# Kernel tuning notes

Measured on AMD Instinct MI355X. Metric: run time of the kernel, lower is better.

## Reference

```python
import jax, jax.numpy as jnp
import numpy as np
from jax import lax

C, H, W, N = 128, 48, 48, 16
SHIFT_W = 1   # frozen value of p_3_1_1 (random.randint(-3,3) in original)
SHIFT_C = 1   # frozen value of p_11_0_1


def setup_inputs() -> dict:
    key = jax.random.key(0)
    k1, k2, k3, k4, k5 = jax.random.split(key, 5)
    x = jax.random.normal(k1, (N, C, H, W), dtype=jnp.float32)
    # p_5_w: trunc_normal std=0.02, shape (1,c,h,w)
    p5_w = 0.02 * jax.random.truncated_normal(k2, -2.0, 2.0, (1, C, H, W), dtype=jnp.float32)
    # p_6: 1x1 conv c->c, no bias -> weight (c, c)
    w6 = jax.random.normal(k3, (C, C), dtype=jnp.float32) / np.float32(np.sqrt(C))
    # p_8: Conv2d(1, c//2, (1,5), dilation=(1,3), padding=(0,6), bias=False)
    w8 = jax.random.normal(k4, (C // 2, 1, 1, 5), dtype=jnp.float32) / np.float32(np.sqrt(5))
    # p_10: 1x1 conv 3c/2 -> c, no bias
    w10 = jax.random.normal(k5, (C, 3 * C // 2), dtype=jnp.float32) / np.float32(np.sqrt(3 * C // 2))
    return {"x": x, "p5_w": p5_w, "w6": w6, "w8": w8, "w10": w10}


def _forward(x, p5_w, w6, w8, w10):
    n, c, h, w = x.shape
    hw = h * w
    inv_sqrt_c = np.float32(1.0 / np.sqrt(c))
    inv_sqrt_hw = np.float32(1.0 / np.sqrt(hw))

    t1 = x.max(axis=1)                                    # (n,h,w) channel max
    t2 = -x
    t4 = jnp.maximum(t2, jnp.roll(t2, SHIFT_W, axis=3))    # roll along width
    t5 = p5_w * t4
    t6 = jnp.einsum('oc,nchw->nohw', w6, t5)               # 1x1 conv p_6

    # score tensor t_7: (n, hw, hw)
    t7 = jnp.einsum('ncp,ncq->npq', t6.reshape(n, c, hw), x.reshape(n, c, hw)) * inv_sqrt_c

    # dilated 1x5 conv on channel-max map
    t8 = lax.conv_general_dilated(
        t1[:, None, :, :], w8, window_strides=(1, 1),
        padding=((0, 0), (6, 6)), rhs_dilation=(1, 3),
        dimension_numbers=('NCHW', 'OIHW', 'NCHW'))        # (n, c/2, h, w)

    # unfold kernel (3,1), dilation (2,1), padding (2,0): rows i-2, i, i+2
    pad = jnp.pad(t8, ((0, 0), (0, 0), (2, 2), (0, 0)))
    t9 = jnp.stack([pad[:, :, 2 * k:2 * k + h, :] for k in range(3)], axis=2)  # (n,c/2,3,h,w)

    t10 = jnp.einsum('oc,nchw->nohw', w10, t9.reshape(n, 3 * c // 2, h, w))   # 1x1 conv p_10
    t11 = jnp.roll(t10, SHIFT_C, axis=1)                   # roll along channels
    t12 = jnp.maximum(x, t11)

    # out[n,q,c] = sum_p t7[n,p,q] * t12[n,c,p]
    t13 = jnp.einsum('npq,ncp->nqc', t7, t12.reshape(n, c, hw)) * inv_sqrt_hw
    return t13.reshape(n, h, w, c).transpose(0, 3, 1, 2)   # (n,c,h,w)


def reference(x, p5_w, w6, w8, w10):
    return _forward(x, p5_w, w6, w8, w10)
```

## Files before the change

### kernel.cpp

```cpp
#include <hip/hip_runtime.h>
#include <cmath>

typedef short bf16x8 __attribute__((ext_vector_type(8)));
typedef short bf16x4 __attribute__((ext_vector_type(4)));
typedef float f32x4 __attribute__((ext_vector_type(4)));

namespace {
constexpr int kN   = 16;
constexpr int kC   = 128;
constexpr int kH   = 48;
constexpr int kW   = 48;
constexpr int kHW  = kH * kW;
constexpr int kK9  = 192;
constexpr int kNPC = 18;
constexpr int kPCH = kHW / kNPC;
constexpr int kLS  = 132;
constexpr int kPA  = 136;
}

__device__ __forceinline__ unsigned short f2b(float f) {
  unsigned u = __builtin_bit_cast(unsigned, f);
  u = (u + 0x7FFFu + ((u >> 16) & 1u)) >> 16;
  return (unsigned short)u;
}
__device__ __forceinline__ float b2f(unsigned short u) {
  return __builtin_bit_cast(float, ((unsigned)u) << 16);
}

__device__ __forceinline__ int tidx(int w, int c) {
  return w * kLS + (c ^ (((w >> 2) & 3) << 3));
}

__global__ __launch_bounds__(256)
void k_prep(const float* __restrict__ p5, const float* __restrict__ w6,
            const float* __restrict__ w10, const float* __restrict__ w8,
            float* __restrict__ p5T, unsigned short* __restrict__ w6b,
            float* __restrict__ Weff) {
  const int tid = threadIdx.x;
  const int bb = blockIdx.x;
  if (bb < 48) {
    __shared__ float Ls[kW * kLS];
    const int h = bb;
    for (int i = 0; i < 6; ++i) {
      const int idx = i * 256 + tid;
      const int c = idx / 12, s = idx % 12;
      const float4 v = *(const float4*)(p5 + (size_t)c * kHW + h * kW + s * 4);
      const int sw = (s & 3) << 3;
      Ls[(4 * s + 0) * kLS + (c ^ sw)] = v.x;
      Ls[(4 * s + 1) * kLS + (c ^ sw)] = v.y;
      Ls[(4 * s + 2) * kLS + (c ^ sw)] = v.z;
      Ls[(4 * s + 3) * kLS + (c ^ sw)] = v.w;
    }
    __syncthreads();
    for (int i = 0; i < 3; ++i) {
      const int idx = i * 256 + tid;
      const int w = idx >> 4, c = (idx & 15) * 8;
      const float* s = &Ls[tidx(w, c)];
      float4 a{s[0], s[1], s[2], s[3]}, b{s[4], s[5], s[6], s[7]};
      float* dst = p5T + ((size_t)(h * kW + w)) * kC + c;
      *(float4*)dst = a;
      *(float4*)(dst + 4) = b;
    }
  } else if (bb < 112) {
    const int i = (bb - 48) * 256 + tid;
    w6b[i] = f2b(w6[i]);
  } else {
    const int idx = (bb - 112) * 256 + tid;
    if (idx < kC * 15) {
      const int o = idx / 15, t = idx - o * 15;
      const int kk = t / 5, j = t - kk * 5;
      float s = 0.f;
#pragma unroll
      for (int c2 = 0; c2 < 64; ++c2)
        s = fmaf(w10[o * kK9 + 3 * c2 + kk], w8[c2 * 5 + j], s);
      Weff[idx] = s;
    }
  }
}

__global__ __launch_bounds__(256)
void k_xt5t6(const float* __restrict__ x, const float* __restrict__ p5T,
             const unsigned short* __restrict__ w6b,
             unsigned short* __restrict__ xT, unsigned short* __restrict__ xB,
             float* __restrict__ t1, unsigned short* __restrict__ t6) {
  __shared__ __align__(16) float Ls[kW * kLS];
  __shared__ __align__(16) unsigned short w6s[kC * kPA];
  __shared__ __align__(16) unsigned short t5s[kW * kPA];
  const int b = blockIdx.x;
  const int n = b / kH, h = b - n * kH;
  const int tid = threadIdx.x;
  const float* xrow = x + (size_t)n * kC * kHW + h * kW;
  unsigned short* xBrow = xB + (size_t)n * kC * kHW + h * kW;
  for (int i = 0; i < 6; ++i) {
    const int idx = i * 256 + tid;
    const int c = idx / 12, s = idx % 12;
    const float4 v = *(const float4*)(xrow + (size_t)c * kHW + s * 4);
    const int sw = (s & 3) << 3;
    Ls[(4 * s + 0) * kLS + (c ^ sw)] = v.x;
    Ls[(4 * s + 1) * kLS + (c ^ sw)] = v.y;
    Ls[(4 * s + 2) * kLS + (c ^ sw)] = v.z;
    Ls[(4 * s + 3) * kLS + (c ^ sw)] = v.w;
    bf16x4 xb4{(short)f2b(v.x), (short)f2b(v.y), (short)f2b(v.z), (short)f2b(v.w)};
    *(bf16x4*)(xBrow + (size_t)c * kHW + s * 4) = xb4;
  }
  for (int i = 0; i < 8; ++i) {
    const int f = i * 256 + tid;
    const int o = f >> 4, seg = (f & 15) * 8;
    *(bf16x8*)&w6s[o * kPA + seg] = *(const bf16x8*)(w6b + o * kC + seg);
  }
  __syncthreads();

  for (int i = 0; i < 3; ++i) {
    const int idx = i * 256 + tid;
    const int w = idx >> 4, c = (idx & 15) * 8;
    const int wp = (w == 0) ? (kW - 1) : (w - 1);
    const float* sv = &Ls[tidx(w, c)];
    const float* sp = &Ls[tidx(wp, c)];
    const int q = h * kW + w;
    const float* pv = p5T + (size_t)q * kC + c;

    unsigned short xb[8], tb[8];
    float m = -3.4e38f;
#pragma unroll
    for (int j = 0; j < 8; ++j) {
      const float xv = sv[j];
      const float t5 = pv[j] * fmaxf(-xv, -sp[j]);
      xb[j] = f2b(xv);
      tb[j] = f2b(t5);
      m = fmaxf(m, xv);
    }
    *(bf16x8*)(xT + ((size_t)n * kHW + q) * kC + c) = *(const bf16x8*)xb;
    *(bf16x8*)&t5s[w * kPA + c] = *(const bf16x8*)tb;
#pragma unroll
    for (int off = 1; off < 16; off <<= 1)
      m = fmaxf(m, __shfl_xor(m, off, 16));
    if ((tid & 15) == 0) t1[(size_t)n * kHW + q] = m;
  }
  __syncthreads();

  const int wv = tid >> 6, lane = tid & 63;
  const int lr = lane & 15, lk = (lane >> 4) * 8;
  f32x4 acc[2][3];
#pragma unroll
  for (int i = 0; i < 2; ++i)
#pragma unroll
    for (int j = 0; j < 3; ++j) acc[i][j] = f32x4{0.f, 0.f, 0.f, 0.f};
#pragma unroll
  for (int ks = 0; ks < kC; ks += 32) {
    bf16x8 a[2], bf[3];
#pragma unroll
    for (int mt = 0; mt < 2; ++mt)
      a[mt] = *(const bf16x8*)&w6s[(32 * wv + 16 * mt + lr) * kPA + ks + lk];
#pragma unroll
    for (int nt = 0; nt < 3; ++nt)
      bf[nt] = *(const bf16x8*)&t5s[(16 * nt + lr) * kPA + ks + lk];
#pragma unroll
    for (int mt = 0; mt < 2; ++mt)
#pragma unroll
      for (int nt = 0; nt < 3; ++nt)
        acc[mt][nt] = __builtin_amdgcn_mfma_f32_16x16x32_bf16(a[mt], bf[nt], acc[mt][nt], 0, 0, 0);
  }
#pragma unroll
  for (int mt = 0; mt < 2; ++mt)
#pragma unroll
    for (int nt = 0; nt < 3; ++nt) {
      const int q = h * kW + 16 * nt + lr;
#pragma unroll
      for (int r = 0; r < 4; ++r) {
        const int o = 32 * wv + 16 * mt + 4 * (lane >> 4) + r;
        t6[((size_t)n * kC + o) * kHW + q] = f2b(acc[mt][nt][r]);
      }
    }
}

__global__ __launch_bounds__(256)
void k_corr(const unsigned short* __restrict__ xB, const float* __restrict__ t1,
            const float* __restrict__ Weff, const unsigned short* __restrict__ t6,
            float* __restrict__ part) {
  __shared__ __align__(16) unsigned short t12s[kC * kPA];
  __shared__ __align__(16) unsigned short Bsf[kC * kPA];
  __shared__ __align__(16) float t1s[8 * 60];
  __shared__ float sW[kC][15];
  const int tid = threadIdx.x;
  const int n = blockIdx.y;
  const int p0 = blockIdx.x * kPCH;
  const int h_lo = p0 / kW;
  const unsigned short* Bg = t6 + (size_t)n * kC * kHW + p0;

  for (int i = tid; i < 8 * 60; i += 256) {
    const int r = i / 60, cc = i - r * 60;
    const int hh = h_lo - 2 + r, ww = cc - 6;
    t1s[i] = (hh >= 0 && hh < kH && ww >= 0 && ww < kW) ? t1[n * kHW + hh * kW + ww] : 0.f;
  }
  for (int i = tid; i < kC * 15; i += 256) {
    const int c = i / 15, t = i - c * 15;
    sW[c][t] = Weff[((c - 1) & (kC - 1)) * 15 + t];
  }
#pragma unroll
  for (int i = 0; i < 8; ++i) {
    const int f = i * 256 + tid;
    const int c = f >> 4, seg = (f & 15) * 8;
    *(bf16x8*)&Bsf[c * kPA + seg] = *(const bf16x8*)(Bg + (size_t)c * kHW + seg);
  }
  __syncthreads();

  const unsigned short* xn = xB + (size_t)n * kC * kHW;
  for (int it = 0; it < 8; ++it) {
    const int idx = it * 256 + tid;
    const int c = idx >> 4, p = (idx & 15) * 8;
    const int q = p0 + p;
    const int h = q / kW, w0 = q - h * kW;
    const int r0 = h - h_lo;
    float tap[3][20];
#pragma unroll
    for (int kk = 0; kk < 3; ++kk) {
      const float* src = &t1s[(r0 + 2 * kk) * 60 + w0];
#pragma unroll
      for (int j4 = 0; j4 < 5; ++j4) {
        const float4 v = *(const float4*)(src + 4 * j4);
        tap[kk][4 * j4 + 0] = v.x; tap[kk][4 * j4 + 1] = v.y;
        tap[kk][4 * j4 + 2] = v.z; tap[kk][4 * j4 + 3] = v.w;
      }
    }
    float wr[15];
#pragma unroll
    for (int t = 0; t < 15; ++t) wr[t] = sW[c][t];
    const bf16x8 xv8 = *(const bf16x8*)(xn + (size_t)c * kHW + q);
    unsigned short o16[8];
#pragma unroll
    for (int dp = 0; dp < 8; ++dp) {
      float acc = 0.f;
#pragma unroll
      for (int kk = 0; kk < 3; ++kk)
#pragma unroll
        for (int j = 0; j < 5; ++j)
          acc = fmaf(wr[kk * 5 + j], tap[kk][3 * j + dp], acc);
      o16[dp] = f2b(fmaxf(b2f((unsigned short)xv8[dp]), acc));
    }
    *(bf16x8*)&t12s[c * kPA + p] = *(const bf16x8*)o16;
  }
  __syncthreads();

  const int wv = tid >> 6, lane = tid & 63;
  const int lr = lane & 15, lk = (lane >> 4) * 8;
  const int wr2 = (wv >> 1) * 64, wc2 = (wv & 1) * 64;
  f32x4 acc[4][4];
#pragma unroll
  for (int i = 0; i < 4; ++i)
#pragma unroll
    for (int j = 0; j < 4; ++j) acc[i][j] = f32x4{0.f, 0.f, 0.f, 0.f};

#pragma unroll
  for (int ks = 0; ks < kPCH; ks += 32) {
    bf16x8 a[4], bv[4];
#pragma unroll
    for (int i = 0; i < 4; ++i) {
      a[i]  = *(const bf16x8*)&t12s[(wr2 + 16 * i + lr) * kPA + ks + lk];
      bv[i] = *(const bf16x8*)&Bsf[(wc2 + 16 * i + lr) * kPA + ks + lk];
    }
#pragma unroll
    for (int i = 0; i < 4; ++i)
#pragma unroll
      for (int j = 0; j < 4; ++j)
        acc[i][j] = __builtin_amdgcn_mfma_f32_16x16x32_bf16(a[i], bv[j], acc[i][j], 0, 0, 0);
  }

  float* dst = part + ((size_t)blockIdx.x * kN + n) * (kC * kC);
#pragma unroll
  for (int i = 0; i < 4; ++i)
#pragma unroll
    for (int j = 0; j < 4; ++j)
#pragma unroll
      for (int r = 0; r < 4; ++r)
        dst[(wr2 + 16 * i + 4 * (lane >> 4) + r) * kC + wc2 + 16 * j + lr] = acc[i][j][r];
}

__global__ __launch_bounds__(256)
void k_redM(const float* __restrict__ part, unsigned short* __restrict__ M) {
  const int idx = blockIdx.x * 256 + threadIdx.x;
  const int n = idx >> 14, r = idx & 16383;
  float s = 0.f;
#pragma unroll
  for (int ch = 0; ch < kNPC; ++ch)
    s += part[(((size_t)ch * kN + n) << 14) + r];
  M[idx] = f2b(s);
}

__global__ __launch_bounds__(256)
void k_out(const unsigned short* __restrict__ A, const unsigned short* __restrict__ B,
           float* __restrict__ Out, float scale) {
  constexpr int K = 128;
  __shared__ __align__(16) unsigned short As[kC * kPA];
  __shared__ __align__(16) unsigned short Bs[64 * kPA];
  const int tid = threadIdx.x;
  const int n = blockIdx.y;
  const int qbase = blockIdx.x * 64;
  const unsigned short* Ag = A + (size_t)n * kC * K;
  const unsigned short* Bg = B + ((size_t)n * kHW + qbase) * K;

  {
    const int m = tid >> 1, hf = tid & 1;
    const unsigned short* src = Ag + (size_t)m * K + hf * 64;
    unsigned short* dst = &As[m * kPA + hf * 64];
#pragma unroll
    for (int i = 0; i < 8; ++i)
      *(bf16x8*)(dst + 8 * i) = *(const bf16x8*)(src + 8 * i);
  }
#pragma unroll
  for (int i = 0; i < 4; ++i) {
    const int f = i * 256 + tid;
    const int q = f >> 4, seg = (f & 15) * 8;
    *(bf16x8*)&Bs[q * kPA + seg] = *(const bf16x8*)(Bg + (size_t)q * K + seg);
  }
  __syncthreads();

  const int wv = tid >> 6, lane = tid & 63;
  const int lr = lane & 15, lk = (lane >> 4) * 8;

  f32x4 acc[2][4];
#pragma unroll
  for (int i = 0; i < 2; ++i)
#pragma unroll
    for (int j = 0; j < 4; ++j) acc[i][j] = f32x4{0.f, 0.f, 0.f, 0.f};

#pragma unroll
  for (int ks = 0; ks < K; ks += 32) {
    bf16x8 a[2], b[4];
#pragma unroll
    for (int mt = 0; mt < 2; ++mt)
      a[mt] = *(const bf16x8*)&As[(32 * wv + 16 * mt + lr) * kPA + ks + lk];
#pragma unroll
    for (int nt = 0; nt < 4; ++nt)
      b[nt] = *(const bf16x8*)&Bs[(16 * nt + lr) * kPA + ks + lk];
#pragma unroll
    for (int mt = 0; mt < 2; ++mt)
#pragma unroll
      for (int nt = 0; nt < 4; ++nt)
        acc[mt][nt] = __builtin_amdgcn_mfma_f32_16x16x32_bf16(
            a[mt], b[nt], acc[mt][nt], 0, 0, 0);
  }

#pragma unroll
  for (int mt = 0; mt < 2; ++mt)
#pragma unroll
    for (int nt = 0; nt < 4; ++nt) {
      const int q = qbase + 16 * nt + lr;
#pragma unroll
      for (int r = 0; r < 4; ++r) {
        const int m = 32 * wv + 16 * mt + 4 * (lane >> 4) + r;
        Out[((size_t)n * kC + m) * kHW + q] = scale * acc[mt][nt][r];
      }
    }
}

extern "C" void kernel_launch(void* const* d_in, const int* in_sizes, int n_in,
                              void* d_out, int out_size, void* d_ws, size_t ws_size,
                              hipStream_t stream) {
  const float* x   = (const float*)d_in[0];
  const float* p5  = (const float*)d_in[1];
  const float* w6  = (const float*)d_in[2];
  const float* w8  = (const float*)d_in[3];
  const float* w10 = (const float*)d_in[4];
  float* out = (float*)d_out;

  char* ws = (char*)d_ws;
  unsigned short* xT   = (unsigned short*)(ws);
  unsigned short* t6b  = (unsigned short*)(ws + 9437184);
  float*          part = (float*)(ws + 18874368);
  unsigned short* xB   = (unsigned short*)(ws + 37748736);
  unsigned short* Mb   = (unsigned short*)(ws + 47185920);
  float*          t1b  = (float*)(ws + 47710208);
  unsigned short* w6b  = (unsigned short*)(ws + 47857664);
  float*          Weff = (float*)(ws + 47890432);
  float*          p5T  = (float*)(ws + 47898112);

  const float scale = 1.0f / (sqrtf((float)kC) * sqrtf((float)kHW));

  k_prep<<<120, 256, 0, stream>>>(p5, w6, w10, w8, p5T, w6b, Weff);
  k_xt5t6<<<kN * kH, 256, 0, stream>>>(x, p5T, w6b, xT, xB, t1b, t6b);
  k_corr<<<dim3(kNPC, kN), 256, 0, stream>>>(xB, t1b, Weff, t6b, part);
  k_redM<<<kN * kC * kC / 256, 256, 0, stream>>>(part, Mb);
  k_out<<<dim3(kHW / 64, kN), 256, 0, stream>>>(Mb, xT, out, scale);
}
```

Measured before the change: 50.12 us.

## Fold prep kernel into first stage, store partials as bf16, remap block order

Removes the separate prep kernel. The first stage now converts w6 to bf16 itself, computes t5 directly from the coalesced x and p5 row loads, and has block 0 compute Weff. Correlation partial sums are stored as bf16 instead of fp32, and the reduction reads them as 8-wide vectors. Grids are flattened with n as the fastest-varying block index, which changes which blocks run together and how they share the cache. Bf16 partials halve the traffic for partials but add rounding error before the sum. Having block 0 compute Weff inside the same kernel is only safe because Weff is consumed by the next launch.

```diff
diff --git a/kernel.cpp b/kernel.cpp
--- a/kernel.cpp
+++ b/kernel.cpp
@@ -32,41 +32,21 @@
 }
 
 __global__ __launch_bounds__(256)
-void k_prep(const float* __restrict__ p5, const float* __restrict__ w6,
-            const float* __restrict__ w10, const float* __restrict__ w8,
-            float* __restrict__ p5T, unsigned short* __restrict__ w6b,
-            float* __restrict__ Weff) {
+void k_xt5t6(const float* __restrict__ x, const float* __restrict__ p5,
+             const float* __restrict__ w6, const float* __restrict__ w10,
+             const float* __restrict__ w8,
+             unsigned short* __restrict__ xT, unsigned short* __restrict__ xB,
+             float* __restrict__ t1, unsigned short* __restrict__ t6,
+             float* __restrict__ Weff) {
+  __shared__ __align__(16) float Ls[kW * kLS];
+  __shared__ __align__(16) unsigned short w6s[kC * kPA];
+  __shared__ __align__(16) unsigned short t5s[kW * kPA];
+  const int bid = blockIdx.x;
+  const int h = bid >> 4, n = bid & 15;
   const int tid = threadIdx.x;
-  const int bb = blockIdx.x;
-  if (bb < 48) {
-    __shared__ float Ls[kW * kLS];
-    const int h = bb;
-    for (int i = 0; i < 6; ++i) {
-      const int idx = i * 256 + tid;
-      const int c = idx / 12, s = idx % 12;
-      const float4 v = *(const float4*)(p5 + (size_t)c * kHW + h * kW + s * 4);
-      const int sw = (s & 3) << 3;
-      Ls[(4 * s + 0) * kLS + (c ^ sw)] = v.x;
-      Ls[(4 * s + 1) * kLS + (c ^ sw)] = v.y;
-      Ls[(4 * s + 2) * kLS + (c ^ sw)] = v.z;
-      Ls[(4 * s + 3) * kLS + (c ^ sw)] = v.w;
-    }
-    __syncthreads();
-    for (int i = 0; i < 3; ++i) {
-      const int idx = i * 256 + tid;
-      const int w = idx >> 4, c = (idx & 15) * 8;
-      const float* s = &Ls[tidx(w, c)];
-      float4 a{s[0], s[1], s[2], s[3]}, b{s[4], s[5], s[6], s[7]};
-      float* dst = p5T + ((size_t)(h * kW + w)) * kC + c;
-      *(float4*)dst = a;
-      *(float4*)(dst + 4) = b;
-    }
-  } else if (bb < 112) {
-    const int i = (bb - 48) * 256 + tid;
-    w6b[i] = f2b(w6[i]);
-  } else {
-    const int idx = (bb - 112) * 256 + tid;
-    if (idx < kC * 15) {
+
+  if (bid == 0) {
+    for (int idx = tid; idx < kC * 15; idx += 256) {
       const int o = idx / 15, t = idx - o * 15;
       const int kk = t / 5, j = t - kk * 5;
       float s = 0.f;
@@ -76,25 +56,17 @@
       Weff[idx] = s;
     }
   }
-}
-
-__global__ __launch_bounds__(256)
-void k_xt5t6(const float* __restrict__ x, const float* __restrict__ p5T,
-             const unsigned short* __restrict__ w6b,
-             unsigned short* __restrict__ xT, unsigned short* __restrict__ xB,
-             float* __restrict__ t1, unsigned short* __restrict__ t6) {
-  __shared__ __align__(16) float Ls[kW * kLS];
-  __shared__ __align__(16) unsigned short w6s[kC * kPA];
-  __shared__ __align__(16) unsigned short t5s[kW * kPA];
-  const int b = blockIdx.x;
-  const int n = b / kH, h = b - n * kH;
-  const int tid = threadIdx.x;
+
   const float* xrow = x + (size_t)n * kC * kHW + h * kW;
+  const float* prow = p5 + h * kW;
   unsigned short* xBrow = xB + (size_t)n * kC * kHW + h * kW;
+
   for (int i = 0; i < 6; ++i) {
     const int idx = i * 256 + tid;
     const int c = idx / 12, s = idx % 12;
     const float4 v = *(const float4*)(xrow + (size_t)c * kHW + s * 4);
+    const float xm1 = xrow[(size_t)c * kHW + ((s == 0) ? (kW - 1) : (s * 4 - 1))];
+    const float4 pv = *(const float4*)(prow + (size_t)c * kHW + s * 4);
     const int sw = (s & 3) << 3;
     Ls[(4 * s + 0) * kLS + (c ^ sw)] = v.x;
     Ls[(4 * s + 1) * kLS + (c ^ sw)] = v.y;
@@ -102,35 +74,40 @@
     Ls[(4 * s + 3) * kLS + (c ^ sw)] = v.w;
     bf16x4 xb4{(short)f2b(v.x), (short)f2b(v.y), (short)f2b(v.z), (short)f2b(v.w)};
     *(bf16x4*)(xBrow + (size_t)c * kHW + s * 4) = xb4;
+    const float t50 = pv.x * fmaxf(-v.x, -xm1);
+    const float t51 = pv.y * fmaxf(-v.y, -v.x);
+    const float t52 = pv.z * fmaxf(-v.z, -v.y);
+    const float t53 = pv.w * fmaxf(-v.w, -v.z);
+    t5s[(4 * s + 0) * kPA + c] = f2b(t50);
+    t5s[(4 * s + 1) * kPA + c] = f2b(t51);
+    t5s[(4 * s + 2) * kPA + c] = f2b(t52);
+    t5s[(4 * s + 3) * kPA + c] = f2b(t53);
   }
   for (int i = 0; i < 8; ++i) {
     const int f = i * 256 + tid;
     const int o = f >> 4, seg = (f & 15) * 8;
-    *(bf16x8*)&w6s[o * kPA + seg] = *(const bf16x8*)(w6b + o * kC + seg);
+    const float4 a = *(const float4*)(w6 + (size_t)o * kC + seg);
+    const float4 b = *(const float4*)(w6 + (size_t)o * kC + seg + 4);
+    bf16x8 w8v{(short)f2b(a.x), (short)f2b(a.y), (short)f2b(a.z), (short)f2b(a.w),
+               (short)f2b(b.x), (short)f2b(b.y), (short)f2b(b.z), (short)f2b(b.w)};
+    *(bf16x8*)&w6s[o * kPA + seg] = w8v;
   }
   __syncthreads();
 
   for (int i = 0; i < 3; ++i) {
     const int idx = i * 256 + tid;
     const int w = idx >> 4, c = (idx & 15) * 8;
-    const int wp = (w == 0) ? (kW - 1) : (w - 1);
     const float* sv = &Ls[tidx(w, c)];
-    const float* sp = &Ls[tidx(wp, c)];
     const int q = h * kW + w;
-    const float* pv = p5T + (size_t)q * kC + c;
-
-    unsigned short xb[8], tb[8];
+    unsigned short xb[8];
     float m = -3.4e38f;
 #pragma unroll
     for (int j = 0; j < 8; ++j) {
       const float xv = sv[j];
-      const float t5 = pv[j] * fmaxf(-xv, -sp[j]);
       xb[j] = f2b(xv);
-      tb[j] = f2b(t5);
       m = fmaxf(m, xv);
     }
     *(bf16x8*)(xT + ((size_t)n * kHW + q) * kC + c) = *(const bf16x8*)xb;
-    *(bf16x8*)&t5s[w * kPA + c] = *(const bf16x8*)tb;
 #pragma unroll
     for (int off = 1; off < 16; off <<= 1)
       m = fmaxf(m, __shfl_xor(m, off, 16));
@@ -176,14 +153,15 @@
 __global__ __launch_bounds__(256)
 void k_corr(const unsigned short* __restrict__ xB, const float* __restrict__ t1,
             const float* __restrict__ Weff, const unsigned short* __restrict__ t6,
-            float* __restrict__ part) {
+            unsigned short* __restrict__ part) {
   __shared__ __align__(16) unsigned short t12s[kC * kPA];
   __shared__ __align__(16) unsigned short Bsf[kC * kPA];
   __shared__ __align__(16) float t1s[8 * 60];
   __shared__ float sW[kC][15];
+  const int bid = blockIdx.x;
+  const int chunk = bid >> 4, n = bid & 15;
   const int tid = threadIdx.x;
-  const int n = blockIdx.y;
-  const int p0 = blockIdx.x * kPCH;
+  const int p0 = chunk * kPCH;
   const int h_lo = p0 / kW;
   const unsigned short* Bg = t6 + (size_t)n * kC * kHW + p0;
 
@@ -265,25 +243,34 @@
         acc[i][j] = __builtin_amdgcn_mfma_f32_16x16x32_bf16(a[i], bv[j], acc[i][j], 0, 0, 0);
   }
 
-  float* dst = part + ((size_t)blockIdx.x * kN + n) * (kC * kC);
+  unsigned short* dst = part + ((size_t)chunk * kN + n) * (kC * kC);
 #pragma unroll
   for (int i = 0; i < 4; ++i)
 #pragma unroll
     for (int j = 0; j < 4; ++j)
 #pragma unroll
       for (int r = 0; r < 4; ++r)
-        dst[(wr2 + 16 * i + 4 * (lane >> 4) + r) * kC + wc2 + 16 * j + lr] = acc[i][j][r];
+        dst[(wr2 + 16 * i + 4 * (lane >> 4) + r) * kC + wc2 + 16 * j + lr] = f2b(acc[i][j][r]);
 }
 
 __global__ __launch_bounds__(256)
-void k_redM(const float* __restrict__ part, unsigned short* __restrict__ M) {
-  const int idx = blockIdx.x * 256 + threadIdx.x;
-  const int n = idx >> 14, r = idx & 16383;
-  float s = 0.f;
-#pragma unroll
-  for (int ch = 0; ch < kNPC; ++ch)
-    s += part[(((size_t)ch * kN + n) << 14) + r];
-  M[idx] = f2b(s);
+void k_redM(const unsigned short* __restrict__ part, unsigned short* __restrict__ M) {
+  const int bid = blockIdx.x;
+  const int j = bid >> 4, n = bid & 15;
+  const int r0 = (j * 256 + threadIdx.x) * 8;
+  float acc[8];
+#pragma unroll
+  for (int e = 0; e < 8; ++e) acc[e] = 0.f;
+#pragma unroll
+  for (int ch = 0; ch < kNPC; ++ch) {
+    const bf16x8 v = *(const bf16x8*)(part + (((size_t)ch * kN + n) << 14) + r0);
+#pragma unroll
+    for (int e = 0; e < 8; ++e) acc[e] += b2f((unsigned short)v[e]);
+  }
+  unsigned short o16[8];
+#pragma unroll
+  for (int e = 0; e < 8; ++e) o16[e] = f2b(acc[e]);
+  *(bf16x8*)(M + ((size_t)n << 14) + r0) = *(const bf16x8*)o16;
 }
 
 __global__ __launch_bounds__(256)
@@ -292,9 +279,10 @@
   constexpr int K = 128;
   __shared__ __align__(16) unsigned short As[kC * kPA];
   __shared__ __align__(16) unsigned short Bs[64 * kPA];
+  const int bid = blockIdx.x;
+  const int qt = bid >> 4, n = bid & 15;
   const int tid = threadIdx.x;
-  const int n = blockIdx.y;
-  const int qbase = blockIdx.x * 64;
+  const int qbase = qt * 64;
   const unsigned short* Ag = A + (size_t)n * kC * K;
   const unsigned short* Bg = B + ((size_t)n * kHW + qbase) * K;
 
@@ -366,19 +354,16 @@
   char* ws = (char*)d_ws;
   unsigned short* xT   = (unsigned short*)(ws);
   unsigned short* t6b  = (unsigned short*)(ws + 9437184);
-  float*          part = (float*)(ws + 18874368);
-  unsigned short* xB   = (unsigned short*)(ws + 37748736);
-  unsigned short* Mb   = (unsigned short*)(ws + 47185920);
-  float*          t1b  = (float*)(ws + 47710208);
-  unsigned short* w6b  = (unsigned short*)(ws + 47857664);
-  float*          Weff = (float*)(ws + 47890432);
-  float*          p5T  = (float*)(ws + 47898112);
+  unsigned short* part = (unsigned short*)(ws + 18874368);
+  unsigned short* xB   = (unsigned short*)(ws + 28311552);
+  unsigned short* Mb   = (unsigned short*)(ws + 37748736);
+  float*          t1b  = (float*)(ws + 38273024);
+  float*          Weff = (float*)(ws + 38420480);
 
   const float scale = 1.0f / (sqrtf((float)kC) * sqrtf((float)kHW));
 
-  k_prep<<<120, 256, 0, stream>>>(p5, w6, w10, w8, p5T, w6b, Weff);
-  k_xt5t6<<<kN * kH, 256, 0, stream>>>(x, p5T, w6b, xT, xB, t1b, t6b);
-  k_corr<<<dim3(kNPC, kN), 256, 0, stream>>>(xB, t1b, Weff, t6b, part);
-  k_redM<<<kN * kC * kC / 256, 256, 0, stream>>>(part, Mb);
-  k_out<<<dim3(kHW / 64, kN), 256, 0, stream>>>(Mb, xT, out, scale);
-}
+  k_xt5t6<<<kN * kH, 256, 0, stream>>>(x, p5, w6, w10, w8, xT, xB, t1b, t6b, Weff);
+  k_corr<<<kNPC * kN, 256, 0, stream>>>(xB, t1b, Weff, t6b, part);
+  k_redM<<<8 * kN, 256, 0, stream>>>(part, Mb);
+  k_out<<<(kHW / 64) * kN, 256, 0, stream>>>(Mb, xT, out, scale);
+}
```

Result: slower. 68.22 us (+36.1%).
